# Performance work log

Measured on AMD Instinct MI355X. Metric: run time of the kernel, lower is better.

Reference implementation:

```python
import jax, jax.numpy as jnp
import numpy as np
from jax import lax

# Shapes / module constants
B, N = 16, 1048576          # batch, events per sample (multiple of S)
H, W = 256, 256             # sensor resolution (init dim)
S = 32                      # temporal segments (hardcoded in forward)
START = 2                   # self.startIdx
SEG = N // S                # events per segment


def setup_inputs() -> dict:
    key = jax.random.key(0)
    k1, k2 = jax.random.split(key)
    xs = jax.random.randint(k1, (B, N), 0, W, dtype=jnp.int32)
    ys = jax.random.randint(k2, (B, N), 0, H, dtype=jnp.int32)
    # self.blurFilterKernel: center 0.5, surround 0.0625 (shared across groups)
    blur_kernel = jnp.array(
        [0.0625, 0.0625, 0.0625, 0.0625, 0.5, 0.0625, 0.0625, 0.0625, 0.0625],
        dtype=jnp.float32).reshape(3, 3)
    return {"xs": xs, "ys": ys, "blur_kernel": blur_kernel}


def _aligned_shift(coord, dimlen, blur_kernel):
    """Per-segment histogram along one spatial axis -> clamp -> blur -> centroid
    alignment. coord: [B, N] int32 in [0, dimlen). Returns [B, S] int32 shifts."""
    chunks = jnp.repeat(jnp.arange(S, dtype=jnp.int32), SEG)      # [N]
    idx = coord + dimlen * chunks[None, :]                         # [B, N]
    hist = jax.vmap(
        lambda i: jnp.zeros(S * dimlen, jnp.int32).at[i].add(1))(idx)
    hist = hist.astype(jnp.float32)                                # [B, S*dimlen]
    mean = hist.mean(axis=-1, keepdims=True)
    std = jnp.std(hist, axis=-1, ddof=1, keepdims=True)            # torch unbiased std
    hist = jnp.clip(hist, 0.0, mean + 3.0 * std)
    img = hist.reshape(B, 1, S, dimlen)
    # grouped conv with identical kernel per group == single-channel conv
    blurred = lax.conv_general_dilated(
        img, blur_kernel.reshape(1, 1, 3, 3), (1, 1), ((1, 1), (1, 1)))
    blurred = blurred.reshape(B, S, dimlen)
    m = jnp.einsum('bsw,w->bs', blurred,
                   jnp.arange(dimlen, dtype=jnp.float32)) / float(SEG)
    start = m[:, START:START + 1]
    # aligned = m - start - (dimlen//2 - start)
    aligned = jnp.round(m - start - (dimlen // 2 - start)).astype(jnp.int32)
    return aligned


def _accumulate(idx_c, idx_v):
    """Adaptive accumulation for one batch element.
    idx_c: [S, SEG] container indices, idx_v: [S, SEG] verifier indices."""
    container = jnp.zeros(W * H, jnp.int32).at[idx_c[START]].add(1)
    verifier = jnp.zeros((W // 2) * (H // 2), bool).at[idx_v[START]].set(True)

    def step(carry, seg):
        cont, ver, active = carry
        ic, iv = seg
        v_new = ver.at[iv].set(True)
        new_cnt = v_new.sum().astype(jnp.float32)
        xor_cnt = jnp.logical_xor(v_new, ver).sum().astype(jnp.float32)
        # original breaks when new_info ratio < 0.01 (segment NOT added)
        proceed = active & (xor_cnt / new_cnt >= 0.01)
        cont = jnp.where(proceed, cont.at[ic].add(1), cont)
        ver = jnp.where(proceed, v_new, ver)
        return (cont, ver, proceed), None

    (container, _, _), _ = lax.scan(
        step, (container, verifier, jnp.bool_(True)),
        (idx_c[START + 1:], idx_v[START + 1:]))
    return container


def _forward(xs, ys, blur_kernel):
    alignedX = _aligned_shift(xs, W, blur_kernel)   # [B, S]
    alignedY = _aligned_shift(ys, H, blur_kernel)   # [B, S]
    shX = jnp.repeat(alignedX, SEG, axis=1)          # [B, N]
    shY = jnp.repeat(alignedY, SEG, axis=1)
    xsft = jnp.clip(xs - shX, 0, W - 1)
    ysft = jnp.clip(ys - shY, 0, H - 1)
    idx_c = (xsft + W * ysft).reshape(B, S, SEG)
    idx_v = (xsft // 2 + (W // 2) * (ysft // 2)).reshape(B, S, SEG)
    containers = jax.vmap(_accumulate)(idx_c, idx_v)  # [B, W*H]
    return containers.reshape(B, 1, H, W).astype(jnp.float32)


def reference(xs, ys, blur_kernel):
    return _forward(xs, ys, blur_kernel)
```

## Files before the change

kernel.cpp:

```cpp
#include <hip/hip_runtime.h>
#include <cstdint>
#include <cstddef>

#define BB 16
#define NTOT 1048576
#define SS 32
#define SEG 32768
#define DIM 256
#define VW 512

#define OFF_HX   0u
#define OFF_HY   524288u
#define OFF_BM0  1048576u
#define OFF_BM1  0u
#define OFF_AX   2097152u
#define OFF_AY   2099200u
#define OFF_PR   2101248u
#define OFF_ACT  2103296u
#define OFF_TOT  2104320u
#define OFF_VER  2105344u
#define OFF_STG  2138112u

__device__ __forceinline__ int clamp255(int v) {
    return v < 0 ? 0 : (v > 255 ? 255 : v);
}

__global__ __launch_bounds__(256) void k_hist4(const int* __restrict__ xs,
                                               const int* __restrict__ ys,
                                               uint32_t* __restrict__ histX,
                                               uint32_t* __restrict__ histY,
                                               uint32_t* __restrict__ staging) {
    int blk = blockIdx.x;
    int arr = blk & 1;
    int s = (blk >> 1) & 31;
    int b = blk >> 6;
    int t = threadIdx.x;
    staging[(size_t)blk * 512 + t] = 0u;
    staging[(size_t)blk * 512 + 256 + t] = 0u;

    const int* src = arr ? ys : xs;
    uint32_t* dst = arr ? histY : histX;
    __shared__ uint32_t ph[256][32];
    uint32_t* phl = (uint32_t*)ph;
#pragma unroll
    for (int i = 0; i < 32; ++i) phl[t + i * 256] = 0u;
    __syncthreads();
    int c = t & 31;
    const int4* p4 = (const int4*)(src + (size_t)b * NTOT + (size_t)s * SEG);
#pragma unroll 8
    for (int i = 0; i < 32; ++i) {
        int4 v = p4[i * 256 + t];
        atomicAdd(&ph[v.x][c], 1u);
        atomicAdd(&ph[v.y][c], 1u);
        atomicAdd(&ph[v.z][c], 1u);
        atomicAdd(&ph[v.w][c], 1u);
    }
    __syncthreads();
    uint32_t sum = 0u;
#pragma unroll
    for (int j = 0; j < 32; ++j)
        sum += ph[t][(j + t) & 31];
    dst[(size_t)(b * SS + s) * 256 + t] = sum;
}

__global__ __launch_bounds__(256) void k_shifts(const uint32_t* __restrict__ histX,
                                                const uint32_t* __restrict__ histY,
                                                const float* __restrict__ blurk,
                                                int* __restrict__ alignedX,
                                                int* __restrict__ alignedY) {
    int blk = blockIdx.x;
    int b = blk >> 1, axis = blk & 1;
    const uint32_t* hist = (axis == 0 ? histX : histY) + (size_t)b * SS * DIM;
    int* out = (axis == 0 ? alignedX : alignedY) + b * SS;

    __shared__ float vals[SS][DIM];
    __shared__ double wsq[4];
    __shared__ float mrow[SS];
    int t = threadIdx.x;
    int w = t >> 6, lane = t & 63;
    int c0 = lane << 2;

    double lsq = 0.0;
    for (int r = w; r < SS; r += 4) {
        uint4 u = *(const uint4*)(hist + r * DIM + c0);
        float v0 = (float)u.x, v1 = (float)u.y, v2 = (float)u.z, v3 = (float)u.w;
        vals[r][c0 + 0] = v0; vals[r][c0 + 1] = v1;
        vals[r][c0 + 2] = v2; vals[r][c0 + 3] = v3;
        double d0 = (double)v0 - 128.0, d1 = (double)v1 - 128.0;
        double d2 = (double)v2 - 128.0, d3 = (double)v3 - 128.0;
        lsq += d0 * d0 + d1 * d1 + d2 * d2 + d3 * d3;
    }
    for (int o = 32; o > 0; o >>= 1) lsq += __shfl_xor(lsq, o, 64);
    if (lane == 0) wsq[w] = lsq;
    __syncthreads();
    float s2 = (float)(wsq[0] + wsq[1] + wsq[2] + wsq[3]);
    float sd = sqrtf(s2 / 8191.0f);
    float thr = 128.0f + 3.0f * sd;

    float k00 = blurk[0], k01 = blurk[1], k02 = blurk[2];
    float k10 = blurk[3], k11 = blurk[4], k12 = blurk[5];
    float k20 = blurk[6], k21 = blurk[7], k22 = blurk[8];

#define V(r, c) fminf(vals[r][c], thr)
    for (int s = w; s < SS; s += 4) {
        double dot = 0.0;
#pragma unroll
        for (int j = 0; j < 4; ++j) {
            int c = c0 + j;
            int cm = c - 1, cp = c + 1;
            bool cml = (cm >= 0), cpl = (cp < DIM);
            float bsum = 0.0f;
            if (s - 1 >= 0) {
                if (cml) bsum += k00 * V(s - 1, cm);
                bsum += k01 * V(s - 1, c);
                if (cpl) bsum += k02 * V(s - 1, cp);
            }
            if (cml) bsum += k10 * V(s, cm);
            bsum += k11 * V(s, c);
            if (cpl) bsum += k12 * V(s, cp);
            if (s + 1 < SS) {
                if (cml) bsum += k20 * V(s + 1, cm);
                bsum += k21 * V(s + 1, c);
                if (cpl) bsum += k22 * V(s + 1, cp);
            }
            dot += (double)bsum * (double)c;
        }
        for (int o = 32; o > 0; o >>= 1) dot += __shfl_xor(dot, o, 64);
        if (lane == 0) mrow[s] = (float)(dot / 32768.0);
    }
#undef V
    __syncthreads();

    if (t < SS) {
        float start = mrow[2];
        float a = mrow[t] - start;
        float c = 128.0f - start;
        out[t] = (int)rintf(a - c);
    }
}

__global__ __launch_bounds__(256) void k_bitmap_g(const int* __restrict__ xs,
                                                  const int* __restrict__ ys,
                                                  const int* __restrict__ aX,
                                                  const int* __restrict__ aY,
                                                  const int* __restrict__ active,
                                                  uint32_t* __restrict__ bmp,
                                                  int first_seg, int nseg,
                                                  int parts, int check_active) {
    int blk = blockIdx.x;
    int p = blk % parts;
    int sl = (blk / parts) % nseg;
    int b = blk / (parts * nseg);
    if (check_active && !active[b]) return;
    int s = first_seg + sl;
    int shx = aX[b * SS + s];
    int shy = aY[b * SS + s];
    __shared__ uint32_t bm[VW];
    int t = threadIdx.x;
    bm[t] = 0u; bm[t + 256] = 0u;
    __syncthreads();
    size_t base = (size_t)b * NTOT + (size_t)s * SEG + (size_t)p * (SEG / parts);
    const int4* x4 = (const int4*)(xs + base);
    const int4* y4 = (const int4*)(ys + base);
    int iters = SEG / (parts * 1024);
    for (int i = 0; i < iters; ++i) {
        int4 xv = x4[i * 256 + t];
        int4 yv = y4[i * 256 + t];
#define DOV(xc, yc) { int xf = clamp255((xc) - shx); int yf = clamp255((yc) - shy); \
                      int iv = (xf >> 1) + ((yf >> 1) << 7); \
                      atomicOr(&bm[iv >> 5], 1u << (iv & 31)); }
        DOV(xv.x, yv.x) DOV(xv.y, yv.y) DOV(xv.z, yv.z) DOV(xv.w, yv.w)
#undef DOV
    }
    __syncthreads();
    uint32_t* outp = bmp + ((size_t)(b * nseg + sl) * parts + p) * VW;
    outp[t] = bm[t];
    outp[t + 256] = bm[t + 256];
}

__global__ __launch_bounds__(256) void k_scan_g(const uint32_t* __restrict__ bmp,
                                                int* __restrict__ proceed,
                                                uint32_t* __restrict__ ver_state,
                                                int* __restrict__ total_state,
                                                int* __restrict__ active_state,
                                                int first_seg, int nseg,
                                                int parts, int do_init) {
    int b = blockIdx.x;
    int t = threadIdx.x;
    __shared__ uint32_t ver[VW];
    __shared__ int wred[4];
    __shared__ int sh_flag;
    __shared__ int sh_total;

    for (int i = t; i < nseg; i += 256) proceed[b * SS + first_seg + i] = 0;

    int active = do_init ? 1 : active_state[b];
    if (!active) {
        if (t == 0) active_state[b] = 0;
        return;
    }

    const uint32_t* base = bmp + (size_t)b * nseg * parts * VW;
    int wid = t >> 6, lane = t & 63;
    int start_local;

    if (do_init) {
        uint32_t w0 = 0, w1 = 0;
        for (int p = 0; p < parts; ++p) {
            w0 |= base[(size_t)p * VW + t];
            w1 |= base[(size_t)p * VW + t + 256];
        }
        ver[t] = w0; ver[t + 256] = w1;
        int c = __popc(w0) + __popc(w1);
        for (int o = 32; o > 0; o >>= 1) c += __shfl_down(c, o, 64);
        if (lane == 0) wred[wid] = c;
        __syncthreads();
        if (t == 0) {
            sh_total = wred[0] + wred[1] + wred[2] + wred[3];
            proceed[b * SS + first_seg] = 1;
        }
        start_local = 1;
    } else {
        ver[t] = ver_state[(size_t)b * VW + t];
        ver[t + 256] = ver_state[(size_t)b * VW + t + 256];
        if (t == 0) sh_total = total_state[b];
        start_local = 0;
    }
    __syncthreads();

    for (int sl = start_local; sl < nseg; ++sl) {
        uint32_t w0 = 0, w1 = 0;
        for (int p = 0; p < parts; ++p) {
            w0 |= base[(size_t)(sl * parts + p) * VW + t];
            w1 |= base[(size_t)(sl * parts + p) * VW + t + 256];
        }
        int c = __popc(w0 & ~ver[t]) + __popc(w1 & ~ver[t + 256]);
        for (int o = 32; o > 0; o >>= 1) c += __shfl_down(c, o, 64);
        if (lane == 0) wred[wid] = c;
        __syncthreads();
        if (t == 0) {
            int newly = wred[0] + wred[1] + wred[2] + wred[3];
            int total = sh_total + newly;
            float ratio = (float)newly / (float)total;
            int f = (ratio >= 0.01f) ? 1 : 0;
            sh_flag = f;
            if (f) {
                sh_total = total;
                proceed[b * SS + first_seg + sl] = 1;
            }
        }
        __syncthreads();
        if (!sh_flag) { active = 0; break; }
        ver[t] |= w0;
        ver[t + 256] |= w1;
        __syncthreads();
    }

    ver_state[(size_t)b * VW + t] = ver[t];
    ver_state[(size_t)b * VW + t + 256] = ver[t + 256];
    if (t == 0) {
        total_state[b] = sh_total;
        active_state[b] = active;
    }
}

__global__ __launch_bounds__(1024) void k_accum6(const int* __restrict__ xs,
                                                 const int* __restrict__ ys,
                                                 const int* __restrict__ aX,
                                                 const int* __restrict__ aY,
                                                 const int* __restrict__ proceed,
                                                 uint32_t* __restrict__ staging) {
    int blk = blockIdx.x;
    int p = blk & 3, half = (blk >> 2) & 1, b = blk >> 3;
    __shared__ uint32_t acc[16384];
    int t = threadIdx.x;
    for (int i = t; i < 16384; i += 1024) acc[i] = 0u;
    __syncthreads();
    int ybase = half << 7;
    for (int s = 2; s < SS; ++s) {
        if (!proceed[b * SS + s]) continue;
        int shx = aX[b * SS + s];
        int shy = aY[b * SS + s];
        size_t base = (size_t)b * NTOT + (size_t)s * SEG + (size_t)p * 8192;
        const int4* x4 = (const int4*)(xs + base);
        const int4* y4 = (const int4*)(ys + base);
#pragma unroll
        for (int i = 0; i < 2; ++i) {
            int4 xv = x4[i * 1024 + t];
            int4 yv = y4[i * 1024 + t];
#define DOC(xc, yc) { int xf = clamp255((xc) - shx); int yf = clamp255((yc) - shy); \
                      if ((yf >> 7) == half) { \
                          int cell = xf + ((yf - ybase) << 8); \
                          atomicAdd(&acc[cell >> 1], 1u << ((cell & 1) << 4)); } }
            DOC(xv.x, yv.x) DOC(xv.y, yv.y) DOC(xv.z, yv.z) DOC(xv.w, yv.w)
#undef DOC
        }
    }
    __syncthreads();
    uint32_t* stg = staging + (size_t)b * 32768 + ((size_t)half << 14);
    for (int i = t; i < 16384; i += 1024) {
        uint32_t w = acc[i];
        if (w) atomicAdd(&stg[i], w);
    }
}

__global__ __launch_bounds__(1024) void k_convert(const uint32_t* __restrict__ staging,
                                                  float* __restrict__ out) {
    int g = blockIdx.x * 1024 + threadIdx.x;
    uint32_t w = staging[g];
    ((float2*)out)[g] = make_float2((float)(w & 0xFFFFu), (float)(w >> 16));
}

extern "C" void kernel_launch(void* const* d_in, const int* in_sizes, int n_in,
                              void* d_out, int out_size, void* d_ws, size_t ws_size,
                              hipStream_t stream) {
    const int* xs = (const int*)d_in[0];
    const int* ys = (const int*)d_in[1];
    const float* blurk = (const float*)d_in[2];
    float* out = (float*)d_out;

    uint8_t* ws = (uint8_t*)d_ws;
    uint32_t* histX = (uint32_t*)(ws + OFF_HX);
    uint32_t* histY = (uint32_t*)(ws + OFF_HY);
    int* aX = (int*)(ws + OFF_AX);
    int* aY = (int*)(ws + OFF_AY);
    int* proceed = (int*)(ws + OFF_PR);
    int* active = (int*)(ws + OFF_ACT);
    int* total = (int*)(ws + OFF_TOT);
    uint32_t* ver = (uint32_t*)(ws + OFF_VER);
    uint32_t* bm0 = (uint32_t*)(ws + OFF_BM0);
    uint32_t* bm1 = (uint32_t*)(ws + OFF_BM1);
    uint32_t* staging = (uint32_t*)(ws + OFF_STG);

    k_hist4<<<BB * SS * 2, 256, 0, stream>>>(xs, ys, histX, histY, staging);
    k_shifts<<<BB * 2, 256, 0, stream>>>(histX, histY, blurk, aX, aY);

    k_bitmap_g<<<BB * 8 * 4, 256, 0, stream>>>(xs, ys, aX, aY, active,
                                               bm0, 2, 8, 4, 0);
    k_scan_g<<<BB, 256, 0, stream>>>(bm0, proceed, ver, total, active, 2, 8, 4, 1);

    k_bitmap_g<<<BB * 22 * 2, 256, 0, stream>>>(xs, ys, aX, aY, active,
                                                bm1, 10, 22, 2, 1);
    k_scan_g<<<BB, 256, 0, stream>>>(bm1, proceed, ver, total, active, 10, 22, 2, 0);

    k_accum6<<<BB * 2 * 4, 1024, 0, stream>>>(xs, ys, aX, aY, proceed, staging);
    k_convert<<<512, 1024, 0, stream>>>(staging, out);
}
```

Measured before the change: 73.44 us.

## Replace speculative tail bitmap pass with sequential early-exit tail kernel

Segments 10..31 used to be handled by a speculative parallel bitmap kernel followed by a scan. They are now processed by one block per batch element, which builds each segment's bitmap in shared memory and stops at the first segment that fails the new-information test. This skips reading events for segments that will never be accumulated, but it serializes the tail onto only 16 blocks, which becomes slow if many segments proceed. The first bitmap pass now uses 2 parts instead of 4, and the accumulate kernel is split into 8 parts per half so each block handles one int4 per thread per segment.

```diff
diff --git a/kernel.cpp b/kernel.cpp
--- a/kernel.cpp
+++ b/kernel.cpp
@@ -12,7 +12,6 @@
 #define OFF_HX   0u
 #define OFF_HY   524288u
 #define OFF_BM0  1048576u
-#define OFF_BM1  0u
 #define OFF_AX   2097152u
 #define OFF_AY   2099200u
 #define OFF_PR   2101248u
@@ -143,15 +142,13 @@
                                                   const int* __restrict__ ys,
                                                   const int* __restrict__ aX,
                                                   const int* __restrict__ aY,
-                                                  const int* __restrict__ active,
                                                   uint32_t* __restrict__ bmp,
                                                   int first_seg, int nseg,
-                                                  int parts, int check_active) {
+                                                  int parts) {
     int blk = blockIdx.x;
     int p = blk % parts;
     int sl = (blk / parts) % nseg;
     int b = blk / (parts * nseg);
-    if (check_active && !active[b]) return;
     int s = first_seg + sl;
     int shx = aX[b * SS + s];
     int shy = aY[b * SS + s];
@@ -184,7 +181,7 @@
                                                 int* __restrict__ total_state,
                                                 int* __restrict__ active_state,
                                                 int first_seg, int nseg,
-                                                int parts, int do_init) {
+                                                int parts) {
     int b = blockIdx.x;
     int t = threadIdx.x;
     __shared__ uint32_t ver[VW];
@@ -193,18 +190,12 @@
     __shared__ int sh_total;
 
     for (int i = t; i < nseg; i += 256) proceed[b * SS + first_seg + i] = 0;
-
-    int active = do_init ? 1 : active_state[b];
-    if (!active) {
-        if (t == 0) active_state[b] = 0;
-        return;
-    }
+    int active = 1;
 
     const uint32_t* base = bmp + (size_t)b * nseg * parts * VW;
     int wid = t >> 6, lane = t & 63;
-    int start_local;
-
-    if (do_init) {
+
+    {
         uint32_t w0 = 0, w1 = 0;
         for (int p = 0; p < parts; ++p) {
             w0 |= base[(size_t)p * VW + t];
@@ -219,16 +210,10 @@
             sh_total = wred[0] + wred[1] + wred[2] + wred[3];
             proceed[b * SS + first_seg] = 1;
         }
-        start_local = 1;
-    } else {
-        ver[t] = ver_state[(size_t)b * VW + t];
-        ver[t + 256] = ver_state[(size_t)b * VW + t + 256];
-        if (t == 0) sh_total = total_state[b];
-        start_local = 0;
-    }
-    __syncthreads();
-
-    for (int sl = start_local; sl < nseg; ++sl) {
+    }
+    __syncthreads();
+
+    for (int sl = 1; sl < nseg; ++sl) {
         uint32_t w0 = 0, w1 = 0;
         for (int p = 0; p < parts; ++p) {
             w0 |= base[(size_t)(sl * parts + p) * VW + t];
@@ -264,14 +249,79 @@
     }
 }
 
-__global__ __launch_bounds__(1024) void k_accum6(const int* __restrict__ xs,
+__global__ __launch_bounds__(256) void k_tail(const int* __restrict__ xs,
+                                              const int* __restrict__ ys,
+                                              const int* __restrict__ aX,
+                                              const int* __restrict__ aY,
+                                              int* __restrict__ proceed,
+                                              const uint32_t* __restrict__ ver_state,
+                                              const int* __restrict__ total_state,
+                                              const int* __restrict__ active_state) {
+    int b = blockIdx.x;
+    int t = threadIdx.x;
+    for (int i = t; i < SS - 10; i += 256) proceed[b * SS + 10 + i] = 0;
+    if (!active_state[b]) return;
+
+    __shared__ uint32_t ver[VW];
+    __shared__ uint32_t bm[VW];
+    __shared__ int wred[4];
+    __shared__ int sh_flag;
+    __shared__ int sh_total;
+    ver[t] = ver_state[(size_t)b * VW + t];
+    ver[t + 256] = ver_state[(size_t)b * VW + t + 256];
+    if (t == 0) sh_total = total_state[b];
+    int wid = t >> 6, lane = t & 63;
+    __syncthreads();
+
+    for (int s = 10; s < SS; ++s) {
+        int shx = aX[b * SS + s];
+        int shy = aY[b * SS + s];
+        bm[t] = 0u; bm[t + 256] = 0u;
+        __syncthreads();
+        const int4* x4 = (const int4*)(xs + (size_t)b * NTOT + (size_t)s * SEG);
+        const int4* y4 = (const int4*)(ys + (size_t)b * NTOT + (size_t)s * SEG);
+        for (int i = 0; i < 32; ++i) {
+            int4 xv = x4[i * 256 + t];
+            int4 yv = y4[i * 256 + t];
+#define DOV(xc, yc) { int xf = clamp255((xc) - shx); int yf = clamp255((yc) - shy); \
+                      int iv = (xf >> 1) + ((yf >> 1) << 7); \
+                      atomicOr(&bm[iv >> 5], 1u << (iv & 31)); }
+            DOV(xv.x, yv.x) DOV(xv.y, yv.y) DOV(xv.z, yv.z) DOV(xv.w, yv.w)
+#undef DOV
+        }
+        __syncthreads();
+        uint32_t w0 = bm[t], w1 = bm[t + 256];
+        int c = __popc(w0 & ~ver[t]) + __popc(w1 & ~ver[t + 256]);
+        for (int o = 32; o > 0; o >>= 1) c += __shfl_down(c, o, 64);
+        if (lane == 0) wred[wid] = c;
+        __syncthreads();
+        if (t == 0) {
+            int newly = wred[0] + wred[1] + wred[2] + wred[3];
+            int total = sh_total + newly;
+            float ratio = (float)newly / (float)total;
+            int f = (ratio >= 0.01f) ? 1 : 0;
+            sh_flag = f;
+            if (f) {
+                sh_total = total;
+                proceed[b * SS + s] = 1;
+            }
+        }
+        __syncthreads();
+        if (!sh_flag) break;
+        ver[t] |= w0;
+        ver[t + 256] |= w1;
+        __syncthreads();
+    }
+}
+
+__global__ __launch_bounds__(1024) void k_accum7(const int* __restrict__ xs,
                                                  const int* __restrict__ ys,
                                                  const int* __restrict__ aX,
                                                  const int* __restrict__ aY,
                                                  const int* __restrict__ proceed,
                                                  uint32_t* __restrict__ staging) {
     int blk = blockIdx.x;
-    int p = blk & 3, half = (blk >> 2) & 1, b = blk >> 3;
+    int p = blk & 7, half = (blk >> 3) & 1, b = blk >> 4;
     __shared__ uint32_t acc[16384];
     int t = threadIdx.x;
     for (int i = t; i < 16384; i += 1024) acc[i] = 0u;
@@ -281,20 +331,15 @@
         if (!proceed[b * SS + s]) continue;
         int shx = aX[b * SS + s];
         int shy = aY[b * SS + s];
-        size_t base = (size_t)b * NTOT + (size_t)s * SEG + (size_t)p * 8192;
-        const int4* x4 = (const int4*)(xs + base);
-        const int4* y4 = (const int4*)(ys + base);
-#pragma unroll
-        for (int i = 0; i < 2; ++i) {
-            int4 xv = x4[i * 1024 + t];
-            int4 yv = y4[i * 1024 + t];
+        size_t base = (size_t)b * NTOT + (size_t)s * SEG + (size_t)p * 4096;
+        int4 xv = ((const int4*)(xs + base))[t];
+        int4 yv = ((const int4*)(ys + base))[t];
 #define DOC(xc, yc) { int xf = clamp255((xc) - shx); int yf = clamp255((yc) - shy); \
                       if ((yf >> 7) == half) { \
                           int cell = xf + ((yf - ybase) << 8); \
                           atomicAdd(&acc[cell >> 1], 1u << ((cell & 1) << 4)); } }
-            DOC(xv.x, yv.x) DOC(xv.y, yv.y) DOC(xv.z, yv.z) DOC(xv.w, yv.w)
+        DOC(xv.x, yv.x) DOC(xv.y, yv.y) DOC(xv.z, yv.z) DOC(xv.w, yv.w)
 #undef DOC
-        }
     }
     __syncthreads();
     uint32_t* stg = staging + (size_t)b * 32768 + ((size_t)half << 14);
@@ -329,20 +374,16 @@
     int* total = (int*)(ws + OFF_TOT);
     uint32_t* ver = (uint32_t*)(ws + OFF_VER);
     uint32_t* bm0 = (uint32_t*)(ws + OFF_BM0);
-    uint32_t* bm1 = (uint32_t*)(ws + OFF_BM1);
     uint32_t* staging = (uint32_t*)(ws + OFF_STG);
 
     k_hist4<<<BB * SS * 2, 256, 0, stream>>>(xs, ys, histX, histY, staging);
     k_shifts<<<BB * 2, 256, 0, stream>>>(histX, histY, blurk, aX, aY);
 
-    k_bitmap_g<<<BB * 8 * 4, 256, 0, stream>>>(xs, ys, aX, aY, active,
-                                               bm0, 2, 8, 4, 0);
-    k_scan_g<<<BB, 256, 0, stream>>>(bm0, proceed, ver, total, active, 2, 8, 4, 1);
-
-    k_bitmap_g<<<BB * 22 * 2, 256, 0, stream>>>(xs, ys, aX, aY, active,
-                                                bm1, 10, 22, 2, 1);
-    k_scan_g<<<BB, 256, 0, stream>>>(bm1, proceed, ver, total, active, 10, 22, 2, 0);
-
-    k_accum6<<<BB * 2 * 4, 1024, 0, stream>>>(xs, ys, aX, aY, proceed, staging);
+    k_bitmap_g<<<BB * 8 * 2, 256, 0, stream>>>(xs, ys, aX, aY, bm0, 2, 8, 2);
+    k_scan_g<<<BB, 256, 0, stream>>>(bm0, proceed, ver, total, active, 2, 8, 2);
+
+    k_tail<<<BB, 256, 0, stream>>>(xs, ys, aX, aY, proceed, ver, total, active);
+
+    k_accum7<<<BB * 2 * 8, 1024, 0, stream>>>(xs, ys, aX, aY, proceed, staging);
     k_convert<<<512, 1024, 0, stream>>>(staging, out);
 }
```

After: 73.79 us. No clear change (+0.5%).
